# Optimization experiments

Hardware: AMD Instinct MI355X
Metric: run time of the kernel (lower is better)

## Reference

```python
import jax, jax.numpy as jnp
import numpy as np

NUM_HEADS = 8
NUM_LAYERS = 4
TOKEN_AMOUNT = 16
TOKEN_SIZE = 256
D_MODEL = 512
D_FF = 2048


def _layernorm(x, g, b, eps=1e-6):
    m = jnp.mean(x, axis=-1, keepdims=True)
    v = jnp.mean((x - m) ** 2, axis=-1, keepdims=True)
    return (x - m) / jnp.sqrt(v + eps) * g + b


def _mha(xq, xkv, W, b, mask, H):
    # W: [4, d, d] (q,k,v,o), b: [4, d]
    B, Tq, d = xq.shape
    Tk = xkv.shape[1]
    dh = d // H
    q = (xq @ W[0] + b[0]).reshape(B, Tq, H, dh).transpose(0, 2, 1, 3)
    k = (xkv @ W[1] + b[1]).reshape(B, Tk, H, dh).transpose(0, 2, 1, 3)
    v = (xkv @ W[2] + b[2]).reshape(B, Tk, H, dh).transpose(0, 2, 1, 3)
    logits = jnp.einsum('bhqd,bhkd->bhqk', q, k) / jnp.sqrt(jnp.float32(dh))
    if mask is not None:
        logits = logits - mask * jnp.finfo(jnp.float32).max
    w = jax.nn.softmax(logits, axis=-1)
    o = jnp.einsum('bhqk,bhkd->bhqd', w, v).transpose(0, 2, 1, 3).reshape(B, Tq, d)
    return o @ W[3] + b[3]


def _pos_enc(T, d):
    i = jnp.arange(d)
    factors = 1.0 / jnp.power(10000.0, (2.0 * (i // 2)).astype(jnp.float32) / d)
    ang = jnp.arange(T, dtype=jnp.float32)[:, None] * factors  # [T, d]
    return jnp.where(i % 2 == 0, jnp.sin(ang), jnp.cos(ang))


def setup_inputs() -> dict:
    key = jax.random.key(0)
    ks = jax.random.split(key, 8)
    B, Lenc, F = 16, 2048, 128
    d, dff, L, TS = D_MODEL, D_FF, NUM_LAYERS, TOKEN_SIZE
    s = 0.02
    return {
        'encoder_output': jax.random.normal(ks[0], (B, Lenc, d), jnp.float32),
        'encoder_input': jax.random.normal(ks[1], (B, Lenc, F), jnp.float32),
        'emb_W': jax.random.normal(ks[2], (TS, d), jnp.float32) * s,
        'emb_b': jnp.zeros((d,), jnp.float32),
        'out_W': jax.random.normal(ks[3], (d, TS), jnp.float32) * s,
        'out_b': jnp.zeros((TS,), jnp.float32),
        'self_W': jax.random.normal(ks[4], (L, 4, d, d), jnp.float32) * s,
        'self_b': jnp.zeros((L, 4, d), jnp.float32),
        'cross_W': jax.random.normal(ks[5], (L, 4, d, d), jnp.float32) * s,
        'cross_b': jnp.zeros((L, 4, d), jnp.float32),
        'ffn_W1': jax.random.normal(ks[6], (L, d, dff), jnp.float32) * s,
        'ffn_b1': jnp.zeros((L, dff), jnp.float32),
        'ffn_W2': jax.random.normal(ks[7], (L, dff, d), jnp.float32) * s,
        'ffn_b2': jnp.zeros((L, d), jnp.float32),
        'ln_g': jnp.ones((L, 3, d), jnp.float32),
        'ln_b': jnp.zeros((L, 3, d), jnp.float32),
    }


def reference(encoder_output, encoder_input, emb_W, emb_b, out_W, out_b,
              self_W, self_b, cross_W, cross_b,
              ffn_W1, ffn_b1, ffn_W2, ffn_b2, ln_g, ln_b):
    B = encoder_output.shape[0]
    d = emb_W.shape[1]
    H = NUM_HEADS
    # padding mask from encoder_input (mask_zero_inputs=True)
    pad_mask = jnp.min((encoder_input == 0).astype(jnp.float32), axis=2)[:, None, None, :]
    tokens = jnp.ones((B, 1, TOKEN_SIZE), dtype=jnp.float32)
    for _ in range(TOKEN_AMOUNT):
        T = tokens.shape[1]
        look_ahead = 1.0 - jnp.tril(jnp.ones((T, T), dtype=jnp.float32))
        tok_pad = jnp.min((tokens == 0).astype(jnp.float32), axis=2)[:, None, None, :]
        la_mask = jnp.maximum(tok_pad, look_ahead)
        x = (tokens @ emb_W + emb_b) * jnp.sqrt(jnp.float32(d)) + _pos_enc(T, d)
        for l in range(NUM_LAYERS):
            a = _mha(x, x, self_W[l], self_b[l], la_mask, H)
            x = _layernorm(x + a, ln_g[l, 0], ln_b[l, 0])
            c = _mha(x, encoder_output, cross_W[l], cross_b[l], pad_mask, H)
            x = _layernorm(x + c, ln_g[l, 1], ln_b[l, 1])
            f = jax.nn.relu(x @ ffn_W1[l] + ffn_b1[l]) @ ffn_W2[l] + ffn_b2[l]
            x = _layernorm(x + f, ln_g[l, 2], ln_b[l, 2])
        next_token = (x @ out_W + out_b)[:, -1:, :]
        tokens = jnp.concatenate([tokens, next_token], axis=1)
    return tokens[:, 1:, :]
```

## Files before the change

### kernel.cpp

```cpp
#include <hip/hip_runtime.h>


typedef unsigned short ushort_t;
typedef __attribute__((ext_vector_type(4))) float f32x4;
typedef __attribute__((ext_vector_type(8))) unsigned short us8;
typedef __attribute__((ext_vector_type(4))) unsigned short us4;

#define NB 256
#define NTHR 1024

__device__ __forceinline__ float bf2f(ushort_t u) {
    union { unsigned int i; float f; } v; v.i = ((unsigned int)u) << 16; return v.f;
}
__device__ __forceinline__ ushort_t f2bf(float f) {
    union { unsigned int i; float f; } v; v.f = f;
    return (ushort_t)((v.i + 0x7FFF + ((v.i >> 16) & 1)) >> 16);
}
__device__ __forceinline__ float wave_sum(float v) {
    #pragma unroll
    for (int m = 32; m; m >>= 1) v += __shfl_xor(v, m);
    return v;
}
__device__ __forceinline__ float wave_max(float v) {
    #pragma unroll
    for (int m = 32; m; m >>= 1) v = fmaxf(v, __shfl_xor(v, m));
    return v;
}

union U64C { unsigned long long u; float2 f; };
__device__ __forceinline__ float clf(const float* p) {
    return __hip_atomic_load(p, __ATOMIC_RELAXED, __HIP_MEMORY_SCOPE_AGENT);
}
__device__ __forceinline__ void csf(float* p, float v) {
    __hip_atomic_store(p, v, __ATOMIC_RELAXED, __HIP_MEMORY_SCOPE_AGENT);
}
__device__ __forceinline__ float2 clf2(const float* p) {
    U64C c; c.u = __hip_atomic_load((unsigned long long*)p, __ATOMIC_RELAXED,
                                    __HIP_MEMORY_SCOPE_AGENT);
    return c.f;
}
__device__ __forceinline__ void csf2(float* p, float x, float y) {
    U64C c; c.f.x = x; c.f.y = y;
    __hip_atomic_store((unsigned long long*)p, c.u, __ATOMIC_RELAXED,
                       __HIP_MEMORY_SCOPE_AGENT);
}

__device__ __forceinline__ void gbar(unsigned* bar, int g) {
    __syncthreads();
    if (threadIdx.x == 0) {
        unsigned* cnt = bar + g * 32;
        unsigned* rel = bar + 512 + g * 32;
        unsigned a = __hip_atomic_fetch_add(cnt, 1u, __ATOMIC_RELAXED,
                                            __HIP_MEMORY_SCOPE_AGENT);
        unsigned e = (a >> 4) + 1u;
        if ((a & 15u) == 15u) {
            __hip_atomic_store(rel, e, __ATOMIC_RELAXED, __HIP_MEMORY_SCOPE_AGENT);
        } else {
            while ((int)(__hip_atomic_load(rel, __ATOMIC_RELAXED,
                                           __HIP_MEMORY_SCOPE_AGENT) - e) < 0)
                __builtin_amdgcn_s_sleep(2);
        }
    }
    __syncthreads();
}

__device__ __forceinline__ void ln512b(const float* __restrict__ row,
                                       const float* __restrict__ g,
                                       const float* __restrict__ be,
                                       int use_ln, float* dst, float* red) {
    int tid = threadIdx.x;
    float a = (tid < 512) ? clf(row + tid) : 0.f;
    if (use_ln) {
        float s = wave_sum(a);
        if ((tid & 63) == 0) red[tid >> 6] = s;
        __syncthreads();
        float tot = 0.f;
        #pragma unroll
        for (int i = 0; i < 16; i++) tot += red[i];
        float mu = tot * (1.f / 512.f);
        float d = (tid < 512) ? (a - mu) : 0.f;
        float v = wave_sum(d * d);
        __syncthreads();
        if ((tid & 63) == 0) red[tid >> 6] = v;
        __syncthreads();
        float vt = 0.f;
        #pragma unroll
        for (int i = 0; i < 16; i++) vt += red[i];
        float rstd = rsqrtf(vt * (1.f / 512.f) + 1e-6f);
        if (tid < 512) dst[tid] = d * rstd * g[tid] + be[tid];
    } else {
        if (tid < 512) dst[tid] = a;
    }
    __syncthreads();
}

template<int NCQ, int K>
__device__ __forceinline__ void gemv_all(const float* xs, const float* __restrict__ W,
                                         int ldw, int col0, float* part) {
    constexpr int S = 1024 / NCQ;
    constexpr int KS = K / S;
    int tid = threadIdx.x;
    int cq = tid & (NCQ - 1), ks = tid / NCQ;
    const float* Wp = W + (size_t)(ks * KS) * ldw + col0 + cq * 4;
    const float* xp = xs + ks * KS;
    f32x4 acc = {0.f, 0.f, 0.f, 0.f};
    #pragma unroll
    for (int r = 0; r < KS; r++)
        acc += xp[r] * *(const f32x4*)(Wp + (size_t)r * ldw);
    #pragma unroll
    for (int m = NCQ; m < 64; m <<= 1) {
        acc[0] += __shfl_xor(acc[0], m);
        acc[1] += __shfl_xor(acc[1], m);
        acc[2] += __shfl_xor(acc[2], m);
        acc[3] += __shfl_xor(acc[3], m);
    }
    int wave = tid >> 6, lane = tid & 63;
    if (lane < NCQ) *(f32x4*)(part + (wave * NCQ + lane) * 4) = acc;
    __syncthreads();
}
template<int NCQ>
__device__ __forceinline__ float gemv_allr(const float* part) {
    float a = 0.f;
    #pragma unroll
    for (int w = 0; w < 16; w++) a += part[w * NCQ * 4 + threadIdx.x];
    return a;
}

struct Args {
    const float *enc, *encIn, *embW, *embB, *outW, *outB;
    const float *selfW, *selfB, *crossW, *crossB;
    const float *fW1, *fb1, *fW2, *fb2, *lng, *lnb;
    float* out;
    unsigned* bar;
    float *x0, *qbuf, *y1, *y2, *y3, *attnb;
    float *lny1, *lny2, *qt, *Pm2, *Ps2, *Pz, *tmpb, *selfK, *selfV;
};


__global__ __launch_bounds__(NTHR, 1) void k_mega(Args A) {
    __shared__ ushort_t encL[65536];
    __shared__ float padL[128];
    __shared__ float sm[6400];
    const int bid = blockIdx.x, tid = threadIdx.x;
    const int b = bid >> 4, r = bid & 15;
    unsigned* bar = A.bar;

    {
        const float* ep = A.enc + ((size_t)b * 2048 + r * 128) * 512;
        #pragma unroll 4
        for (int it = 0; it < 16; it++) {
            int idx = tid + it * 1024;
            float4 v = *(const float4*)(ep + (size_t)idx * 4);
            us4 o; o[0] = f2bf(v.x); o[1] = f2bf(v.y); o[2] = f2bf(v.z); o[3] = f2bf(v.w);
            *(us4*)(encL + idx * 4) = o;
        }
        int key = tid >> 3, sub = tid & 7;
        const float* p = A.encIn + ((size_t)b * 2048 + r * 128 + key) * 128 + sub * 16;
        int ok = 1;
        #pragma unroll
        for (int j = 0; j < 4; j++) {
            float4 v = *(const float4*)(p + j * 4);
            ok &= (v.x == 0.f) & (v.y == 0.f) & (v.z == 0.f) & (v.w == 0.f);
        }
        ok &= __shfl_xor(ok, 1); ok &= __shfl_xor(ok, 2); ok &= __shfl_xor(ok, 4);
        if (sub == 0) padL[key] = ok ? 1.f : 0.f;
    }
    __syncthreads();

    for (int t = 0; t < 16; t++) {
        {
            float* tok = sm;
            float* part = sm + 256;
            if (tid < 256)
                tok[tid] = (t == 0) ? 1.f
                         : clf(A.out + (size_t)b * 4096 + (t - 1) * 256 + tid);
            __syncthreads();
            gemv_all<8, 256>(tok, A.embW, 512, r * 32, part);
            if (tid < 32) {
                float acc = gemv_allr<8>(part);
                int col = r * 32 + tid;
                float expo = (2.0f * (float)(col >> 1)) * (1.f / 512.f);
                float ang = (float)t * powf(10000.0f, -expo);
                float pv = (col & 1) ? cosf(ang) : sinf(ang);
                csf(A.x0 + (size_t)b * 512 + col,
                    (acc + A.embB[col]) * 22.627416997969522f + pv);
            }
        }
        gbar(bar, b);

        for (int l = 0; l < 4; l++) {
            const float* src = (l == 0) ? A.x0 : A.y3;
            const float* gP = (l == 0) ? nullptr : A.lng + ((l - 1) * 3 + 2) * 512;
            const float* bP = (l == 0) ? nullptr : A.lnb + ((l - 1) * 3 + 2) * 512;
            int ulnP = (l != 0);

            {
                float* xs = sm;
                float* red = sm + 512;
                float* part = sm + 1024;
                ln512b(src + (size_t)b * 512, gP, bP, ulnP, xs, red);
                int cq = tid & 7, ks = tid >> 3;
                const float* xp = xs + ks * 4;
                f32x4 a0 = {0.f,0.f,0.f,0.f}, a1 = a0, a2 = a0;
                const float* W0 = A.selfW + ((size_t)(l * 4 + 0)) * 262144
                                + (size_t)(ks * 4) * 512 + r * 32 + cq * 4;
                const float* W1 = W0 + 262144;
                const float* W2 = W1 + 262144;
                #pragma unroll
                for (int rr = 0; rr < 4; rr++) {
                    float x = xp[rr];
                    a0 += x * *(const f32x4*)(W0 + (size_t)rr * 512);
                    a1 += x * *(const f32x4*)(W1 + (size_t)rr * 512);
                    a2 += x * *(const f32x4*)(W2 + (size_t)rr * 512);
                }
                #pragma unroll
                for (int m = 8; m < 64; m <<= 1) {
                    #pragma unroll
                    for (int j = 0; j < 4; j++) {
                        a0[j] += __shfl_xor(a0[j], m);
                        a1[j] += __shfl_xor(a1[j], m);
                        a2[j] += __shfl_xor(a2[j], m);
                    }
                }
                int wave = tid >> 6, lane = tid & 63;
                if (lane < 8) {
                    *(f32x4*)(part + (wave * 8 + lane) * 4) = a0;
                    *(f32x4*)(part + 512 + (wave * 8 + lane) * 4) = a1;
                    *(f32x4*)(part + 1024 + (wave * 8 + lane) * 4) = a2;
                }
                __syncthreads();
                if (tid < 96) {
                    int m = tid >> 5, j = tid & 31;
                    float a = 0.f;
                    #pragma unroll
                    for (int w = 0; w < 16; w++) a += part[m * 512 + w * 32 + j];
                    int col = r * 32 + j;
                    a += A.selfB[(l * 4 + m) * 512 + col];
                    if (m == 0) csf(A.qbuf + (size_t)b * 512 + col, a);
                    else if (m == 1)
                        csf(A.selfK + (((size_t)l * 16 + b) * 16 + t) * 512 + col, a);
                    else
                        csf(A.selfV + (((size_t)l * 16 + b) * 16 + t) * 512 + col, a);
                }
            }
            gbar(bar, b);

            {
                float* xr = sm;
                float* qs = sm + 512;
                float* as2 = sm + 1024;
                float* lg = sm + 2048;
                float* red = sm + 2176;
                float* part = sm + 2560;
                ln512b(src + (size_t)b * 512, gP, bP, ulnP, xr, red);
                if (tid < 256) {
                    float2 v = clf2(A.qbuf + (size_t)b * 512 + tid * 2);
                    qs[tid * 2] = v.x; qs[tid * 2 + 1] = v.y;
                }
                __syncthreads();
                const float* Kb = A.selfK + ((size_t)l * 16 + b) * 16 * 512;
                const float* Vb = A.selfV + ((size_t)l * 16 + b) * 16 * 512;
                if (tid < 512) {
                    int idx = tid >> 2, q4 = tid & 3;
                    int h = idx >> 4, j = idx & 15;
                    if (j <= t) {
                        const float* kp = Kb + (size_t)j * 512 + h * 64 + q4 * 16;
                        const float* qp = qs + h * 64 + q4 * 16;
                        float s = 0.f;
                        #pragma unroll
                        for (int d = 0; d < 16; d += 2) {
                            float2 kv = clf2(kp + d);
                            s += qp[d] * kv.x + qp[d + 1] * kv.y;
                        }
                        s += __shfl_xor(s, 1);
                        s += __shfl_xor(s, 2);
                        if (q4 == 0) lg[h * 16 + j] = s * 0.125f;
                    }
                }
                __syncthreads();
                if (tid < 8) {
                    float m = -1e30f;
                    for (int j = 0; j <= t; j++) m = fmaxf(m, lg[tid * 16 + j]);
                    float ssum = 0.f;
                    for (int j = 0; j <= t; j++) {
                        float e = __expf(lg[tid * 16 + j] - m);
                        lg[tid * 16 + j] = e; ssum += e;
                    }
                    float inv = 1.f / ssum;
                    for (int j = 0; j <= t; j++) lg[tid * 16 + j] *= inv;
                }
                __syncthreads();
                {
                    int col = tid & 511, jh = tid >> 9;
                    float a = 0.f;
                    for (int j = jh; j <= t; j += 2)
                        a += lg[(col >> 6) * 16 + j] * clf(Vb + (size_t)j * 512 + col);
                    as2[jh * 512 + col] = a;
                }
                __syncthreads();
                if (tid < 512) qs[tid] = as2[tid] + as2[512 + tid];
                __syncthreads();
                gemv_all<8, 512>(qs, A.selfW + ((size_t)(l * 4 + 3)) * 262144,
                                 512, r * 32, part);
                if (tid < 32) {
                    int col = r * 32 + tid;
                    csf(A.y1 + (size_t)b * 512 + col,
                        gemv_allr<8>(part) + A.selfB[(l * 4 + 3) * 512 + col] + xr[col]);
                }
            }
            gbar(bar, b);

            {
                int h = r >> 1, half = r & 1;
                float* xsw = sm;
                float* red = sm + 512;
                float* qch = sm + 544;
                float* part = sm + 1024;
                ln512b(A.y1 + (size_t)b * 512, A.lng + (l * 3) * 512,
                       A.lnb + (l * 3) * 512, 1, xsw, red);
                if (r == 0 && tid < 512)
                    csf(A.lny1 + (size_t)b * 512 + tid, xsw[tid]);
                gemv_all<16, 512>(xsw, A.crossW + ((size_t)(l * 4)) * 262144,
                                  512, h * 64, part);
                if (tid < 64)
                    qch[tid] = gemv_allr<16>(part)
                             + A.crossB[(l * 4) * 512 + h * 64 + tid];
                __syncthreads();
                {
                    int D = half * 256 + (tid >> 2), q4 = tid & 3;
                    const float* wr = A.crossW + ((size_t)(l * 4 + 1)) * 262144
                                    + (size_t)D * 512 + h * 64 + q4 * 16;
                    const float* qp = qch + q4 * 16;
                    float a = 0.f;
                    #pragma unroll
                    for (int j = 0; j < 16; j += 4) {
                        f32x4 wv = *(const f32x4*)(wr + j);
                        a += qp[j]*wv[0] + qp[j+1]*wv[1] + qp[j+2]*wv[2] + qp[j+3]*wv[3];
                    }
                    a += __shfl_xor(a, 1);
                    a += __shfl_xor(a, 2);
                    if (q4 == 0)
                        csf(A.qt + ((size_t)b * 8 + h) * 512 + D, a * 0.125f);
                }
            }
            gbar(bar, b);

            {
                float* qts = sm;
                float* lge = sm + 4160;
                float* wms = sm + 5184;
                float* wss = sm + 5200;
                #pragma unroll
                for (int it = 0; it < 2; it++) {
                    int p = (tid + it * 1024) * 2;
                    float2 v = clf2(A.qt + (size_t)b * 4096 + p);
                    int row = p >> 9, d = p & 511;
                    qts[row * 520 + d] = v.x;
                    qts[row * 520 + d + 1] = v.y;
                }
                __syncthreads();
                #pragma unroll
                for (int it = 0; it < 4; it++) {
                    int key = it * 32 + (tid >> 5);
                    int hh = (tid >> 2) & 7, pq = tid & 3;
                    const ushort_t* er = encL + key * 512;
                    const float* q = qts + hh * 520;
                    float a0 = 0.f, a1 = 0.f;
                    #pragma unroll
                    for (int ch = 0; ch < 16; ch++) {
                        int c8 = (pq + ch * 4) * 8;
                        us8 ev8 = *(const us8*)(er + c8);
                        const float* qp = q + c8;
                        a0 += bf2f(ev8[0])*qp[0] + bf2f(ev8[1])*qp[1]
                            + bf2f(ev8[2])*qp[2] + bf2f(ev8[3])*qp[3];
                        a1 += bf2f(ev8[4])*qp[4] + bf2f(ev8[5])*qp[5]
                            + bf2f(ev8[6])*qp[6] + bf2f(ev8[7])*qp[7];
                    }
                    float acc = a0 + a1;
                    acc += __shfl_xor(acc, 1);
                    acc += __shfl_xor(acc, 2);
                    if (pq == 0)
                        lge[hh * 128 + key] = (padL[key] != 0.f) ? -2e30f : acc;
                }
                __syncthreads();
                {
                    int hh = tid >> 7, k = tid & 127;
                    float lv = lge[hh * 128 + k];
                    float mv = wave_max(lv);
                    if ((tid & 63) == 0) wms[tid >> 6] = mv;
                    __syncthreads();
                    float m = fmaxf(wms[hh * 2], wms[hh * 2 + 1]);
                    float ev = __expf(lv - m);
                    float sv = wave_sum(ev);
                    if ((tid & 63) == 0) wss[tid >> 6] = sv;
                    lge[hh * 128 + k] = ev;
                    __syncthreads();
                    if (tid < 8) {
                        int bc = b * 16 + r;
                        csf(A.Pm2 + bc * 8 + tid, fmaxf(wms[tid * 2], wms[tid * 2 + 1]));
                        csf(A.Ps2 + bc * 8 + tid, wss[tid * 2] + wss[tid * 2 + 1]);
                    }
                }
                __syncthreads();
                {
                    int hz = tid >> 7, ii = tid & 127;
                    f32x4 z = {0.f, 0.f, 0.f, 0.f};
                    const ushort_t* ep2 = encL + ii * 4;
                    const float* le = lge + hz * 128;
                    #pragma unroll 4
                    for (int k = 0; k < 128; k++) {
                        float ev = le[k];
                        us4 e4 = *(const us4*)(ep2 + k * 512);
                        z[0] += ev * bf2f(e4[0]); z[1] += ev * bf2f(e4[1]);
                        z[2] += ev * bf2f(e4[2]); z[3] += ev * bf2f(e4[3]);
                    }
                    float* dst = A.Pz + ((size_t)((b * 16 + r) * 8 + hz)) * 512 + ii * 4;
                    csf2(dst, z[0], z[1]);
                    csf2(dst + 2, z[2], z[3]);
                }
            }
            gbar(bar, b);

            {
                int h = r >> 1, half = r & 1;
                float* zs = sm;
                float* zs2 = sm + 512;
                float* ecs = sm + 2560;
                float* part = sm + 2624;
                if (tid < 16) {
                    float mcv = clf(A.Pm2 + (b * 16 + tid) * 8 + h);
                    float mm = mcv;
                    mm = fmaxf(mm, __shfl_xor(mm, 1));
                    mm = fmaxf(mm, __shfl_xor(mm, 2));
                    mm = fmaxf(mm, __shfl_xor(mm, 4));
                    mm = fmaxf(mm, __shfl_xor(mm, 8));
                    float ec = __expf(mcv - mm);
                    float sv = ec * clf(A.Ps2 + (b * 16 + tid) * 8 + h);
                    sv += __shfl_xor(sv, 1); sv += __shfl_xor(sv, 2);
                    sv += __shfl_xor(sv, 4); sv += __shfl_xor(sv, 8);
                    ecs[tid] = ec;
                    if (tid == 0) ecs[16] = 1.f / sv;
                }
                __syncthreads();
                {
                    int cp = (tid & 255) * 2, qtr = tid >> 8;
                    float a0 = 0.f, a1 = 0.f;
                    #pragma unroll
                    for (int j = 0; j < 4; j++) {
                        int cc = qtr * 4 + j;
                        float2 v = clf2(A.Pz + ((size_t)(b * 16 + cc) * 8 + h) * 512 + cp);
                        a0 += ecs[cc] * v.x; a1 += ecs[cc] * v.y;
                    }
                    zs2[qtr * 512 + cp] = a0;
                    zs2[qtr * 512 + cp + 1] = a1;
                }
                __syncthreads();
                if (tid < 512)
                    zs[tid] = (zs2[tid] + zs2[512 + tid] + zs2[1024 + tid]
                             + zs2[1536 + tid]) * ecs[16];
                __syncthreads();
                gemv_all<8, 512>(zs, A.crossW + ((size_t)(l * 4 + 2)) * 262144,
                                 512, h * 64 + half * 32, part);
                if (tid < 32) {
                    int col = h * 64 + half * 32 + tid;
                    csf(A.attnb + (size_t)b * 512 + col,
                        gemv_allr<8>(part) + A.crossB[(l * 4 + 2) * 512 + col]);
                }
            }
            gbar(bar, b);

            {
                float* xa = sm;
                float* part = sm + 512;
                if (tid < 256) {
                    float2 v = clf2(A.attnb + (size_t)b * 512 + tid * 2);
                    xa[tid * 2] = v.x; xa[tid * 2 + 1] = v.y;
                }
                __syncthreads();
                gemv_all<8, 512>(xa, A.crossW + ((size_t)(l * 4 + 3)) * 262144,
                                 512, r * 32, part);
                if (tid < 32) {
                    int col = r * 32 + tid;
                    csf(A.y2 + (size_t)b * 512 + col,
                        gemv_allr<8>(part) + A.crossB[(l * 4 + 3) * 512 + col]
                        + clf(A.lny1 + (size_t)b * 512 + col));
                }
            }
            gbar(bar, b);

            {
                float* xsw = sm;
                float* red = sm + 512;
                float* part = sm + 1024;
                ln512b(A.y2 + (size_t)b * 512, A.lng + (l * 3 + 1) * 512,
                       A.lnb + (l * 3 + 1) * 512, 1, xsw, red);
                if (r == 0 && tid < 512)
                    csf(A.lny2 + (size_t)b * 512 + tid, xsw[tid]);
                gemv_all<32, 512>(xsw, A.fW1 + (size_t)l * 512 * 2048,
                                  2048, r * 128, part);
                if (tid < 128) {
                    int col = r * 128 + tid;
                    csf(A.tmpb + (size_t)b * 2048 + col,
                        fmaxf(gemv_allr<32>(part) + A.fb1[l * 2048 + col], 0.f));
                }
            }
            gbar(bar, b);

            {
                float* ts = sm;
                float* part = sm + 2048;
                {
                    float2 v = clf2(A.tmpb + (size_t)b * 2048 + tid * 2);
                    ts[tid * 2] = v.x; ts[tid * 2 + 1] = v.y;
                }
                __syncthreads();
                gemv_all<8, 2048>(ts, A.fW2 + (size_t)l * 2048 * 512,
                                  512, r * 32, part);
                if (tid < 32) {
                    int col = r * 32 + tid;
                    csf(A.y3 + (size_t)b * 512 + col,
                        gemv_allr<8>(part) + A.fb2[l * 512 + col]
                        + clf(A.lny2 + (size_t)b * 512 + col));
                }
            }
            gbar(bar, b);
        }

        {
            float* xsw = sm;
            float* red = sm + 512;
            float* part = sm + 1024;
            ln512b(A.y3 + (size_t)b * 512, A.lng + 11 * 512, A.lnb + 11 * 512,
                   1, xsw, red);
            gemv_all<4, 512>(xsw, A.outW, 256, r * 16, part);
            if (tid < 16) {
                int col = r * 16 + tid;
                csf(A.out + (size_t)b * 4096 + t * 256 + col,
                    gemv_allr<4>(part) + A.outB[col]);
            }
        }
        gbar(bar, b);
    }
}


extern "C" void kernel_launch(void* const* d_in, const int* in_sizes, int n_in,
                              void* d_out, int out_size, void* d_ws, size_t ws_size,
                              hipStream_t stream) {
    Args A;
    A.enc    = (const float*)d_in[0];
    A.encIn  = (const float*)d_in[1];
    A.embW   = (const float*)d_in[2];
    A.embB   = (const float*)d_in[3];
    A.outW   = (const float*)d_in[4];
    A.outB   = (const float*)d_in[5];
    A.selfW  = (const float*)d_in[6];
    A.selfB  = (const float*)d_in[7];
    A.crossW = (const float*)d_in[8];
    A.crossB = (const float*)d_in[9];
    A.fW1    = (const float*)d_in[10];
    A.fb1    = (const float*)d_in[11];
    A.fW2    = (const float*)d_in[12];
    A.fb2    = (const float*)d_in[13];
    A.lng    = (const float*)d_in[14];
    A.lnb    = (const float*)d_in[15];
    A.out    = (float*)d_out;

    char* ws = (char*)d_ws;
    size_t off = 0;
    auto alloc = [&](size_t bytes) -> char* {
        char* p = ws + off;
        off = (off + bytes + 255) & ~(size_t)255;
        return p;
    };
    char* barrier = alloc(4096);
    A.bar = (unsigned*)barrier;
    A.x0    = (float*)alloc(16 * 512 * 4);
    A.qbuf  = (float*)alloc(16 * 512 * 4);
    A.y1    = (float*)alloc(16 * 512 * 4);
    A.y2    = (float*)alloc(16 * 512 * 4);
    A.y3    = (float*)alloc(16 * 512 * 4);
    A.attnb = (float*)alloc(16 * 512 * 4);
    A.lny1  = (float*)alloc(16 * 512 * 4);
    A.lny2  = (float*)alloc(16 * 512 * 4);
    A.qt    = (float*)alloc((size_t)16 * 8 * 512 * 4);
    A.Pm2   = (float*)alloc(16 * 16 * 8 * 4);
    A.Ps2   = (float*)alloc(16 * 16 * 8 * 4);
    A.Pz    = (float*)alloc((size_t)16 * 16 * 8 * 512 * 4);
    A.tmpb  = (float*)alloc((size_t)16 * 2048 * 4);
    A.selfK = (float*)alloc((size_t)4 * 16 * 16 * 512 * 4);
    A.selfV = (float*)alloc((size_t)4 * 16 * 16 * 512 * 4);
    if (off > ws_size) return;

    hipMemsetAsync(barrier, 0, 4096, stream);
    k_mega<<<dim3(NB), dim3(NTHR), 0, stream>>>(A);
}
```

Baseline: 5.116 ms.

## Swizzle encoder LDS tile and restructure cross-attention logits and PV loops

```diff
diff --git a/kernel.cpp b/kernel.cpp
--- a/kernel.cpp
+++ b/kernel.cpp
@@ -58,7 +58,7 @@
         } else {
             while ((int)(__hip_atomic_load(rel, __ATOMIC_RELAXED,
                                            __HIP_MEMORY_SCOPE_AGENT) - e) < 0)
-                __builtin_amdgcn_s_sleep(2);
+                __builtin_amdgcn_s_sleep(1);
         }
     }
     __syncthreads();
@@ -71,23 +71,21 @@
     int tid = threadIdx.x;
     float a = (tid < 512) ? clf(row + tid) : 0.f;
     if (use_ln) {
-        float s = wave_sum(a);
-        if ((tid & 63) == 0) red[tid >> 6] = s;
+        float s = a, s2 = a * a;
+        #pragma unroll
+        for (int m = 32; m; m >>= 1) {
+            s  += __shfl_xor(s, m);
+            s2 += __shfl_xor(s2, m);
+        }
+        if ((tid & 63) == 0) { red[tid >> 6] = s; red[16 + (tid >> 6)] = s2; }
         __syncthreads();
-        float tot = 0.f;
+        float ts = 0.f, ts2 = 0.f;
         #pragma unroll
-        for (int i = 0; i < 16; i++) tot += red[i];
-        float mu = tot * (1.f / 512.f);
-        float d = (tid < 512) ? (a - mu) : 0.f;
-        float v = wave_sum(d * d);
-        __syncthreads();
-        if ((tid & 63) == 0) red[tid >> 6] = v;
-        __syncthreads();
-        float vt = 0.f;
-        #pragma unroll
-        for (int i = 0; i < 16; i++) vt += red[i];
-        float rstd = rsqrtf(vt * (1.f / 512.f) + 1e-6f);
-        if (tid < 512) dst[tid] = d * rstd * g[tid] + be[tid];
+        for (int i = 0; i < 8; i++) { ts += red[i]; ts2 += red[16 + i]; }
+        float mu = ts * (1.f / 512.f);
+        float var = ts2 * (1.f / 512.f) - mu * mu;
+        float rstd = rsqrtf(var + 1e-6f);
+        if (tid < 512) dst[tid] = (a - mu) * rstd * g[tid] + be[tid];
     } else {
         if (tid < 512) dst[tid] = a;
     }
@@ -138,7 +136,7 @@
 
 
 __global__ __launch_bounds__(NTHR, 1) void k_mega(Args A) {
-    __shared__ ushort_t encL[65536];
+    __shared__ ushort_t encL[128 * 520];
     __shared__ float padL[128];
     __shared__ float sm[6400];
     const int bid = blockIdx.x, tid = threadIdx.x;
@@ -150,9 +148,13 @@
         #pragma unroll 4
         for (int it = 0; it < 16; it++) {
             int idx = tid + it * 1024;
-            float4 v = *(const float4*)(ep + (size_t)idx * 4);
+            int key = idx >> 7;
+            int d = (idx & 127) * 4;
+            int dq = d >> 6, cch = (d >> 3) & 7, lo = d & 7;
+            int phys = key * 520 + dq * 64 + ((cch + dq) & 7) * 8 + lo;
+            float4 v = *(const float4*)(ep + (size_t)key * 512 + d);
             us4 o; o[0] = f2bf(v.x); o[1] = f2bf(v.y); o[2] = f2bf(v.z); o[3] = f2bf(v.w);
-            *(us4*)(encL + idx * 4) = o;
+            *(us4*)(encL + phys) = o;
         }
         int key = tid >> 3, sub = tid & 7;
         const float* p = A.encIn + ((size_t)b * 2048 + r * 128 + key) * 128 + sub * 16;
@@ -346,46 +348,66 @@
             gbar(bar, b);
 
             {
-                float* qts = sm;
-                float* lge = sm + 4160;
-                float* wms = sm + 5184;
-                float* wss = sm + 5200;
+                float* qts3 = sm;
+                float* lge  = sm + 4352;
+                float* wms  = sm + 5440;
+                float* wss  = sm + 5456;
                 #pragma unroll
                 for (int it = 0; it < 2; it++) {
-                    int p = (tid + it * 1024) * 2;
-                    float2 v = clf2(A.qt + (size_t)b * 4096 + p);
-                    int row = p >> 9, d = p & 511;
-                    qts[row * 520 + d] = v.x;
-                    qts[row * 520 + d + 1] = v.y;
-                }
-                __syncthreads();
-                #pragma unroll
-                for (int it = 0; it < 4; it++) {
-                    int key = it * 32 + (tid >> 5);
-                    int hh = (tid >> 2) & 7, pq = tid & 3;
-                    const ushort_t* er = encL + key * 512;
-                    const float* q = qts + hh * 520;
-                    float a0 = 0.f, a1 = 0.f;
-                    #pragma unroll
-                    for (int ch = 0; ch < 16; ch++) {
-                        int c8 = (pq + ch * 4) * 8;
-                        us8 ev8 = *(const us8*)(er + c8);
-                        const float* qp = q + c8;
-                        a0 += bf2f(ev8[0])*qp[0] + bf2f(ev8[1])*qp[1]
-                            + bf2f(ev8[2])*qp[2] + bf2f(ev8[3])*qp[3];
-                        a1 += bf2f(ev8[4])*qp[4] + bf2f(ev8[5])*qp[5]
-                            + bf2f(ev8[6])*qp[6] + bf2f(ev8[7])*qp[7];
-                    }
-                    float acc = a0 + a1;
-                    acc += __shfl_xor(acc, 1);
-                    acc += __shfl_xor(acc, 2);
-                    if (pq == 0)
-                        lge[hh * 128 + key] = (padL[key] != 0.f) ? -2e30f : acc;
+                    int p = tid + it * 1024;
+                    float2 v = clf2(A.qt + (size_t)b * 4096 + p * 2);
+                    int e0 = p * 2;
+                    int hh = e0 >> 9, D = e0 & 511;
+                    int dq = D >> 6, c = (D >> 3) & 7, j = D & 7;
+                    float* dst = qts3 + (dq * 8 + hh) * 68 + c * 8 + j;
+                    dst[0] = v.x; dst[1] = v.y;
+                }
+                __syncthreads();
+                {
+                    int ko = tid >> 6, dq = (tid >> 3) & 7;
+                    int lane = tid & 63;
+                    const float* qb = qts3 + lane * 68;
+                    f32x4 q4[16];
+                    #pragma unroll
+                    for (int c = 0; c < 8; c++) {
+                        q4[2 * c]     = *(const f32x4*)(qb + c * 8);
+                        q4[2 * c + 1] = *(const f32x4*)(qb + c * 8 + 4);
+                    }
+                    float a[8];
+                    #pragma unroll
+                    for (int ki = 0; ki < 8; ki++) a[ki] = 0.f;
+                    #pragma unroll
+                    for (int ki = 0; ki < 8; ki++) {
+                        int key = ko * 8 + ki;
+                        const ushort_t* er = encL + key * 520 + dq * 64;
+                        #pragma unroll
+                        for (int c = 0; c < 8; c++) {
+                            us8 e = *(const us8*)(er + ((c + dq) & 7) * 8);
+                            a[ki] += q4[2*c][0]*bf2f(e[0]) + q4[2*c][1]*bf2f(e[1])
+                                   + q4[2*c][2]*bf2f(e[2]) + q4[2*c][3]*bf2f(e[3])
+                                   + q4[2*c+1][0]*bf2f(e[4]) + q4[2*c+1][1]*bf2f(e[5])
+                                   + q4[2*c+1][2]*bf2f(e[6]) + q4[2*c+1][3]*bf2f(e[7]);
+                        }
+                    }
+                    #pragma unroll
+                    for (int ki = 0; ki < 8; ki++) {
+                        a[ki] += __shfl_xor(a[ki], 8);
+                        a[ki] += __shfl_xor(a[ki], 16);
+                        a[ki] += __shfl_xor(a[ki], 32);
+                    }
+                    if (dq == 0) {
+                        int hh = tid & 7;
+                        #pragma unroll
+                        for (int ki = 0; ki < 8; ki++) {
+                            int key = ko * 8 + ki;
+                            lge[hh * 132 + key] = (padL[key] != 0.f) ? -2e30f : a[ki];
+                        }
+                    }
                 }
                 __syncthreads();
                 {
                     int hh = tid >> 7, k = tid & 127;
-                    float lv = lge[hh * 128 + k];
+                    float lv = lge[hh * 132 + k];
                     float mv = wave_max(lv);
                     if ((tid & 63) == 0) wms[tid >> 6] = mv;
                     __syncthreads();
@@ -393,7 +415,7 @@
                     float ev = __expf(lv - m);
                     float sv = wave_sum(ev);
                     if ((tid & 63) == 0) wss[tid >> 6] = sv;
-                    lge[hh * 128 + k] = ev;
+                    lge[hh * 132 + k] = ev;
                     __syncthreads();
                     if (tid < 8) {
                         int bc = b * 16 + r;
@@ -403,20 +425,37 @@
                 }
                 __syncthreads();
                 {
-                    int hz = tid >> 7, ii = tid & 127;
-                    f32x4 z = {0.f, 0.f, 0.f, 0.f};
-                    const ushort_t* ep2 = encL + ii * 4;
-                    const float* le = lge + hz * 128;
+                    int ii8 = tid >> 4, kh = (tid >> 3) & 1, hz = tid & 7;
+                    int dq = ii8 >> 3, c = ii8 & 7;
+                    const ushort_t* ep2 = encL + dq * 64 + ((c + dq) & 7) * 8;
+                    const float* le = lge + hz * 132 + kh * 64;
+                    f32x4 z0 = {0.f,0.f,0.f,0.f}, z1 = z0;
                     #pragma unroll 4
-                    for (int k = 0; k < 128; k++) {
-                        float ev = le[k];
-                        us4 e4 = *(const us4*)(ep2 + k * 512);
-                        z[0] += ev * bf2f(e4[0]); z[1] += ev * bf2f(e4[1]);
-                        z[2] += ev * bf2f(e4[2]); z[3] += ev * bf2f(e4[3]);
-                    }
-                    float* dst = A.Pz + ((size_t)((b * 16 + r) * 8 + hz)) * 512 + ii * 4;
-                    csf2(dst, z[0], z[1]);
-                    csf2(dst + 2, z[2], z[3]);
+                    for (int k4 = 0; k4 < 16; k4++) {
+                        f32x4 ev4 = *(const f32x4*)(le + k4 * 4);
+                        #pragma unroll
+                        for (int j = 0; j < 4; j++) {
+                            int key = kh * 64 + k4 * 4 + j;
+                            us8 e = *(const us8*)(ep2 + key * 520);
+                            float ev = ev4[j];
+                            z0[0] += ev * bf2f(e[0]); z0[1] += ev * bf2f(e[1]);
+                            z0[2] += ev * bf2f(e[2]); z0[3] += ev * bf2f(e[3]);
+                            z1[0] += ev * bf2f(e[4]); z1[1] += ev * bf2f(e[5]);
+                            z1[2] += ev * bf2f(e[6]); z1[3] += ev * bf2f(e[7]);
+                        }
+                    }
+                    #pragma unroll
+                    for (int j = 0; j < 4; j++) {
+                        z0[j] += __shfl_xor(z0[j], 8);
+                        z1[j] += __shfl_xor(z1[j], 8);
+                    }
+                    if (kh == 0) {
+                        float* dst = A.Pz + ((size_t)((b * 16 + r) * 8 + hz)) * 512 + ii8 * 8;
+                        csf2(dst,     z0[0], z0[1]);
+                        csf2(dst + 2, z0[2], z0[3]);
+                        csf2(dst + 4, z1[0], z1[1]);
+                        csf2(dst + 6, z1[2], z1[3]);
+                    }
                 }
             }
             gbar(bar, b);
```

New measurement: 13.88 ms. 171% more time.
